# Optimization experiments

Hardware: AMD Instinct MI355X
Metric: run time of the kernel (lower is better)

The kernel has to match this reference:

```python
import jax, jax.numpy as jnp
import numpy as np

B, T, C = 32, 1024, 1024
N_LAYER, LAYER_ID, FIRST_SA = 12, 3, 1
RWKV_K_CLAMP = 60.0
RWKV_K_EPS = 1e-16


def _init_params():
    # decay_speed init exactly as in RWKV_TimeMix.__init__
    f1 = 3.0 + (LAYER_ID - FIRST_SA) / (N_LAYER - 1 - FIRST_SA) * (1.2 - 3.0)
    f2 = 0.65 + (LAYER_ID - FIRST_SA) / (N_LAYER - 1 - FIRST_SA) * (0.4 - 0.65)
    h = np.arange(C, dtype=np.float64)
    decay_speed = np.power(f2, h / (C - 1) * 7) * f1
    time_decay = np.log(decay_speed).astype(np.float32)          # (C,)
    time_first = np.full((C,), np.log(0.3), dtype=np.float32)     # (C,)
    tm = np.ones((C,), dtype=np.float32)
    tm[: C // 2] = 0.0                                            # time_mix
    return jnp.asarray(time_decay), jnp.asarray(time_first), jnp.asarray(tm)


def setup_inputs() -> dict:
    key = jax.random.key(0)
    ks = jax.random.split(key, 5)
    x = jax.random.normal(ks[0], (B, T, C), dtype=jnp.float32)
    scale = 0.02
    Wk = jax.random.normal(ks[1], (C, C), dtype=jnp.float32) * scale
    Wv = jax.random.normal(ks[2], (C, C), dtype=jnp.float32) * scale
    Wr = jax.random.normal(ks[3], (C, C), dtype=jnp.float32) * scale
    Wo = jax.random.normal(ks[4], (C, C), dtype=jnp.float32) * scale
    time_decay, time_first, time_mix = _init_params()
    return {"x": x, "time_decay": time_decay, "time_first": time_first,
            "time_mix": time_mix, "Wk": Wk, "Wv": Wv, "Wr": Wr, "Wo": Wo}


def _wkv(decay, first_w, y, eps):
    # out[b,t,c] = eps + first_w[c]*y[b,t,c] + sum_{u<t} decay[c]^(t-1-u) * y[b,u,c]
    # computed as a linear recurrence S[t] = decay*S[t-1] + y[t] via associative scan.
    a = jnp.broadcast_to(decay, y.shape)
    def comb(l, r):
        a1, b1 = l
        a2, b2 = r
        return (a1 * a2, a2 * b1 + b2)
    _, S = jax.lax.associative_scan(comb, (a, y), axis=1)
    S_prev = jnp.pad(S, ((0, 0), (1, 0), (0, 0)))[:, :-1]  # S[t-1], S[-1]=0
    return eps + first_w * y + S_prev


def reference(x, time_decay, time_first, time_mix, Wk, Wv, Wr, Wo):
    Bn, Tn, Cn = x.shape
    # time shift: ZeroPad2d((0,0,1,-1)) -> shifted[t] = x[t-1], shifted[0]=0
    xs = jnp.pad(x, ((0, 0), (1, 0), (0, 0)))[:, :-1]
    xm = x * time_mix + xs * (1.0 - time_mix)
    k = xm @ Wk.T
    v = xm @ Wv.T
    r = xm @ Wr.T
    k = jnp.exp(jnp.minimum(k, RWKV_K_CLAMP))
    kv = k * v
    decay = jnp.exp(-jnp.exp(time_decay))   # lag-d weight (d>=1): decay^(d-1)
    first_w = jnp.exp(time_first)           # lag-0 weight
    wkv = _wkv(decay, first_w, kv, 0.0)
    wk = _wkv(decay, first_w, k, RWKV_K_EPS)
    rwkv = jax.nn.sigmoid(r) * (wkv / wk)
    return rwkv @ Wo.T
```

## Files before the change

### kernel.cpp

```cpp
#include <hip/hip_runtime.h>


#define DEV __device__ __forceinline__

constexpr int Bc = 32, Tc = 1024, Cc = 1024;
constexpr int Mdim = Bc * Tc;
constexpr int Ndim = Cc;
constexpr int Kdim = Cc;
constexpr int NT = Kdim / 64;
constexpr int CHUNK = 128;
constexpr int LOOKB = 128;
constexpr int NCH = Tc / CHUNK;

typedef short bf16x8 __attribute__((ext_vector_type(8)));
typedef float f32x4  __attribute__((ext_vector_type(4)));

DEV unsigned short f2bf(float f) {
    unsigned u = __float_as_uint(f);
    u += 0x7FFFu + ((u >> 16) & 1u);
    return (unsigned short)(u >> 16);
}
DEV float bf2f(unsigned short s) { return __uint_as_float(((unsigned)s) << 16); }

DEV void gload16(const unsigned short* g, const unsigned short* l) {
    __builtin_amdgcn_global_load_lds(
        (const __attribute__((address_space(1))) void*)g,
        (__attribute__((address_space(3))) void*)l, 16, 0, 0);
}

__global__ void wconv_kernel(const float* __restrict__ src, unsigned short* __restrict__ dst) {
    int i = blockIdx.x * blockDim.x + threadIdx.x;
    float4 v = ((const float4*)src)[i];
    ((ushort4*)dst)[i] = make_ushort4(f2bf(v.x), f2bf(v.y), f2bf(v.z), f2bf(v.w));
}

__global__ void xm_kernel(const float* __restrict__ x, const float* __restrict__ tm,
                          unsigned short* __restrict__ xm) {
    int i4 = blockIdx.x * blockDim.x + threadIdx.x;
    int c4 = i4 & (Cc / 4 - 1);
    int t  = (i4 >> 8) & (Tc - 1);
    float4 xc = ((const float4*)x)[i4];
    float4 xp = make_float4(0.f, 0.f, 0.f, 0.f);
    if (t > 0) xp = ((const float4*)x)[i4 - Cc / 4];
    float4 tv = ((const float4*)tm)[c4];
    ushort4 o = make_ushort4(
        f2bf(xc.x * tv.x + xp.x * (1.f - tv.x)),
        f2bf(xc.y * tv.y + xp.y * (1.f - tv.y)),
        f2bf(xc.z * tv.z + xp.z * (1.f - tv.z)),
        f2bf(xc.w * tv.w + xp.w * (1.f - tv.w)));
    ((ushort4*)xm)[i4] = o;
}

template <int MODE>
__global__ __launch_bounds__(512, 2) void gemm256_kernel(
    const unsigned short* __restrict__ A,
    const unsigned short* __restrict__ W,
    void* __restrict__ out)
{
    __shared__ unsigned short lds[2 * 32768];

    const int tid = threadIdx.x;
    const int l = tid & 63, w = tid >> 6;
    const int wr = w >> 2, wc = w & 3;
    const int l15 = l & 15, l4 = l >> 4;
    const size_t row0 = (size_t)blockIdx.x * 256;
    const int col0 = blockIdx.y * 256;

    const int rs = tid >> 3;
    const int cs = ((tid & 7) ^ ((tid >> 3) & 7)) << 3;
    const int swz = (l15 & 7) << 3;

    f32x4 acc[8][4];
#pragma unroll
    for (int m = 0; m < 8; m++)
#pragma unroll
        for (int n = 0; n < 4; n++)
#pragma unroll
            for (int q = 0; q < 4; q++) acc[m][n][q] = 0.f;

#define STAGE(kt, bb) {                                                                \
    _Pragma("unroll")                                                                  \
    for (int g = 0; g < 4; g++)                                                        \
        gload16(A + (row0 + g * 64 + rs) * (size_t)Kdim + (kt) + cs,                   \
                lds + (bb) * 32768 + g * 4096 + w * 512);                              \
    _Pragma("unroll")                                                                  \
    for (int g = 0; g < 4; g++)                                                        \
        gload16(W + (size_t)(col0 + g * 64 + rs) * Kdim + (kt) + cs,                   \
                lds + (bb) * 32768 + 16384 + g * 4096 + w * 512); }

    STAGE(0, 0)
    asm volatile("s_waitcnt vmcnt(0)" ::: "memory");
    __builtin_amdgcn_s_barrier();

    for (int t = 0; t < NT; t++) {
        const int b = t & 1;
        const unsigned short* Ab = lds + b * 32768;
        const unsigned short* Bb = Ab + 16384;
        bf16x8 af0[4][2], af1[4][2], bf0[2][2], bf1[2][2];

#pragma unroll
        for (int mi = 0; mi < 4; mi++)
#pragma unroll
            for (int kk = 0; kk < 2; kk++)
                af0[mi][kk] = *(const bf16x8*)(Ab + (wr * 128 + mi * 16 + l15) * 64 + ((kk * 32 + l4 * 8) ^ swz));
#pragma unroll
        for (int n = 0; n < 2; n++)
#pragma unroll
            for (int kk = 0; kk < 2; kk++)
                bf0[n][kk] = *(const bf16x8*)(Bb + (wc * 64 + n * 16 + l15) * 64 + ((kk * 32 + l4 * 8) ^ swz));
        if (t < NT - 1) STAGE((t + 1) * 64, b ^ 1)
        __builtin_amdgcn_s_barrier();
        asm volatile("s_waitcnt lgkmcnt(0)" ::: "memory");
        __builtin_amdgcn_s_setprio(1);
#pragma unroll
        for (int mi = 0; mi < 4; mi++)
#pragma unroll
            for (int n = 0; n < 2; n++)
#pragma unroll
                for (int kk = 0; kk < 2; kk++)
                    acc[mi][n] = __builtin_amdgcn_mfma_f32_16x16x32_bf16(af0[mi][kk], bf0[n][kk], acc[mi][n], 0, 0, 0);
        __builtin_amdgcn_s_setprio(0);

#pragma unroll
        for (int n = 0; n < 2; n++)
#pragma unroll
            for (int kk = 0; kk < 2; kk++)
                bf1[n][kk] = *(const bf16x8*)(Bb + (wc * 64 + (2 + n) * 16 + l15) * 64 + ((kk * 32 + l4 * 8) ^ swz));
        __builtin_amdgcn_s_barrier();
        asm volatile("s_waitcnt lgkmcnt(0)" ::: "memory");
        __builtin_amdgcn_s_setprio(1);
#pragma unroll
        for (int mi = 0; mi < 4; mi++)
#pragma unroll
            for (int n = 0; n < 2; n++)
#pragma unroll
                for (int kk = 0; kk < 2; kk++)
                    acc[mi][2 + n] = __builtin_amdgcn_mfma_f32_16x16x32_bf16(af0[mi][kk], bf1[n][kk], acc[mi][2 + n], 0, 0, 0);
        __builtin_amdgcn_s_setprio(0);

#pragma unroll
        for (int mi = 0; mi < 4; mi++)
#pragma unroll
            for (int kk = 0; kk < 2; kk++)
                af1[mi][kk] = *(const bf16x8*)(Ab + (wr * 128 + (4 + mi) * 16 + l15) * 64 + ((kk * 32 + l4 * 8) ^ swz));
        __builtin_amdgcn_s_barrier();
        asm volatile("s_waitcnt lgkmcnt(0)" ::: "memory");
        __builtin_amdgcn_s_setprio(1);
#pragma unroll
        for (int mi = 0; mi < 4; mi++)
#pragma unroll
            for (int n = 0; n < 2; n++)
#pragma unroll
                for (int kk = 0; kk < 2; kk++)
                    acc[4 + mi][n] = __builtin_amdgcn_mfma_f32_16x16x32_bf16(af1[mi][kk], bf0[n][kk], acc[4 + mi][n], 0, 0, 0);
        __builtin_amdgcn_s_setprio(0);

        if (t < NT - 1) { asm volatile("s_waitcnt vmcnt(0)" ::: "memory"); }
        __builtin_amdgcn_s_barrier();
        __builtin_amdgcn_s_setprio(1);
#pragma unroll
        for (int mi = 0; mi < 4; mi++)
#pragma unroll
            for (int n = 0; n < 2; n++)
#pragma unroll
                for (int kk = 0; kk < 2; kk++)
                    acc[4 + mi][2 + n] = __builtin_amdgcn_mfma_f32_16x16x32_bf16(af1[mi][kk], bf1[n][kk], acc[4 + mi][2 + n], 0, 0, 0);
        __builtin_amdgcn_s_setprio(0);
    }
#undef STAGE

#pragma unroll
    for (int m = 0; m < 8; m++)
#pragma unroll
        for (int n = 0; n < 4; n++)
#pragma unroll
            for (int q = 0; q < 4; q++) {
                size_t row = row0 + wr * 128 + m * 16 + l4 * 4 + q;
                int col = col0 + wc * 64 + n * 16 + l15;
                size_t idx = row * Ndim + col;
                float v = acc[m][n][q];
                if constexpr (MODE == 0)
                    ((unsigned short*)out)[idx] = f2bf(__expf(fminf(v, 60.f)));
                else if constexpr (MODE == 1)
                    ((unsigned short*)out)[idx] = f2bf(v);
                else if constexpr (MODE == 2)
                    ((unsigned short*)out)[idx] = f2bf(1.f / (1.f + __expf(-v)));
                else
                    ((float*)out)[idx] = v;
            }
}

__global__ __launch_bounds__(256) void scan_kernel(
    const unsigned short* __restrict__ kexp, const unsigned short* __restrict__ vb,
    const unsigned short* __restrict__ sr,
    const float* __restrict__ td, const float* __restrict__ tf,
    unsigned short* __restrict__ rwkv)
{
    int c = blockIdx.x * blockDim.x + threadIdx.x;
    int ch = blockIdx.y;
    int b  = blockIdx.z;
    int t0 = ch * CHUNK;
    int tstart = t0 - LOOKB; if (tstart < 0) tstart = 0;

    float decay = __expf(-__expf(td[c]));
    float fw = __expf(tf[c]);
    float Skv = 0.f, Sk = 0.f;

    size_t base = (size_t)b * Tc * Cc + c;
    size_t idx = base + (size_t)tstart * Cc;
#pragma unroll 8
    for (int t = tstart; t < t0; t++, idx += Cc) {
        float kk = bf2f(kexp[idx]);
        float y  = kk * bf2f(vb[idx]);
        Skv = decay * Skv + y;
        Sk  = decay * Sk  + kk;
    }
#pragma unroll 8
    for (int t = t0; t < t0 + CHUNK; t++, idx += Cc) {
        float kk = bf2f(kexp[idx]);
        float y  = kk * bf2f(vb[idx]);
        float wkv = fw * y + Skv;
        float wk  = 1e-16f + fw * kk + Sk;
        float sig = bf2f(sr[idx]);
        rwkv[idx] = f2bf(sig * (wkv / wk));
        Skv = decay * Skv + y;
        Sk  = decay * Sk  + kk;
    }
}

extern "C" void kernel_launch(void* const* d_in, const int* in_sizes, int n_in,
                              void* d_out, int out_size, void* d_ws, size_t ws_size,
                              hipStream_t stream) {
    const float* x  = (const float*)d_in[0];
    const float* td = (const float*)d_in[1];
    const float* tf = (const float*)d_in[2];
    const float* tm = (const float*)d_in[3];
    const float* Wk = (const float*)d_in[4];
    const float* Wv = (const float*)d_in[5];
    const float* Wr = (const float*)d_in[6];
    const float* Wo = (const float*)d_in[7];

    const size_t BTC = (size_t)Bc * Tc * Cc;
    const size_t WN  = (size_t)Cc * Cc;

    char* ws = (char*)d_ws;
    unsigned short* wkb   = (unsigned short*)ws; ws += WN * 2;
    unsigned short* wvb   = (unsigned short*)ws; ws += WN * 2;
    unsigned short* wrb   = (unsigned short*)ws; ws += WN * 2;
    unsigned short* wob   = (unsigned short*)ws; ws += WN * 2;
    unsigned short* xm    = (unsigned short*)ws; ws += BTC * 2;
    unsigned short* kexpb = (unsigned short*)ws; ws += BTC * 2;
    unsigned short* vbb   = (unsigned short*)ws; ws += BTC * 2;
    unsigned short* srb   = (unsigned short*)ws; ws += BTC * 2;
    float* outp = (float*)d_out;

    wconv_kernel<<<WN / 1024, 256, 0, stream>>>(Wk, wkb);
    wconv_kernel<<<WN / 1024, 256, 0, stream>>>(Wv, wvb);
    wconv_kernel<<<WN / 1024, 256, 0, stream>>>(Wr, wrb);
    wconv_kernel<<<WN / 1024, 256, 0, stream>>>(Wo, wob);

    xm_kernel<<<BTC / 4 / 256, 256, 0, stream>>>(x, tm, xm);

    dim3 ggrid(Mdim / 256, Ndim / 256);
    gemm256_kernel<0><<<ggrid, 512, 0, stream>>>(xm, wkb, (void*)kexpb);
    gemm256_kernel<1><<<ggrid, 512, 0, stream>>>(xm, wvb, (void*)vbb);
    gemm256_kernel<2><<<ggrid, 512, 0, stream>>>(xm, wrb, (void*)srb);

    scan_kernel<<<dim3(Cc / 256, NCH, Bc), 256, 0, stream>>>(kexpb, vbb, srb, td, tf, xm);

    gemm256_kernel<3><<<ggrid, 512, 0, stream>>>(xm, wob, (void*)outp);
}
```

Before: 447.8 us.

## Merge weight conversions, swap GEMM grid order, vectorize scan to two channels per thread

Folds the four weight-conversion launches into one launch using a 2D grid. Swaps the GEMM grid so blockIdx.x walks the 4 column tiles, which means consecutive blocks share the same A row tile and should reuse it in L2. Rewrites the scan so each thread handles two adjacent channels with ushort2 loads and stores, in 64-thread blocks. The scan change widens memory accesses but doubles the register state per thread and halves the thread count.

```diff
diff --git a/kernel.cpp b/kernel.cpp
--- a/kernel.cpp
+++ b/kernel.cpp
@@ -28,8 +28,13 @@
         (__attribute__((address_space(3))) void*)l, 16, 0, 0);
 }
 
-__global__ void wconv_kernel(const float* __restrict__ src, unsigned short* __restrict__ dst) {
+__global__ void wconv_kernel(const float* __restrict__ w0, const float* __restrict__ w1,
+                             const float* __restrict__ w2, const float* __restrict__ w3,
+                             unsigned short* __restrict__ d0, unsigned short* __restrict__ d1,
+                             unsigned short* __restrict__ d2, unsigned short* __restrict__ d3) {
     int i = blockIdx.x * blockDim.x + threadIdx.x;
+    const float* src = (blockIdx.y == 0) ? w0 : (blockIdx.y == 1) ? w1 : (blockIdx.y == 2) ? w2 : w3;
+    unsigned short* dst = (blockIdx.y == 0) ? d0 : (blockIdx.y == 1) ? d1 : (blockIdx.y == 2) ? d2 : d3;
     float4 v = ((const float4*)src)[i];
     ((ushort4*)dst)[i] = make_ushort4(f2bf(v.x), f2bf(v.y), f2bf(v.z), f2bf(v.w));
 }
@@ -63,8 +68,8 @@
     const int l = tid & 63, w = tid >> 6;
     const int wr = w >> 2, wc = w & 3;
     const int l15 = l & 15, l4 = l >> 4;
-    const size_t row0 = (size_t)blockIdx.x * 256;
-    const int col0 = blockIdx.y * 256;
+    const size_t row0 = (size_t)blockIdx.y * 256;
+    const int col0 = blockIdx.x * 256;
 
     const int rs = tid >> 3;
     const int cs = ((tid & 7) ^ ((tid >> 3) & 7)) << 3;
@@ -190,41 +195,50 @@
             }
 }
 
-__global__ __launch_bounds__(256) void scan_kernel(
+__global__ __launch_bounds__(64) void scan_kernel(
     const unsigned short* __restrict__ kexp, const unsigned short* __restrict__ vb,
     const unsigned short* __restrict__ sr,
     const float* __restrict__ td, const float* __restrict__ tf,
     unsigned short* __restrict__ rwkv)
 {
-    int c = blockIdx.x * blockDim.x + threadIdx.x;
+    int c = (blockIdx.x * blockDim.x + threadIdx.x) * 2;
     int ch = blockIdx.y;
     int b  = blockIdx.z;
     int t0 = ch * CHUNK;
     int tstart = t0 - LOOKB; if (tstart < 0) tstart = 0;
 
-    float decay = __expf(-__expf(td[c]));
-    float fw = __expf(tf[c]);
-    float Skv = 0.f, Sk = 0.f;
+    float d0 = __expf(-__expf(td[c]));
+    float d1 = __expf(-__expf(td[c + 1]));
+    float f0 = __expf(tf[c]);
+    float f1 = __expf(tf[c + 1]);
+    float Skv0 = 0.f, Sk0 = 0.f, Skv1 = 0.f, Sk1 = 0.f;
 
     size_t base = (size_t)b * Tc * Cc + c;
     size_t idx = base + (size_t)tstart * Cc;
-#pragma unroll 8
+#pragma unroll 4
     for (int t = tstart; t < t0; t++, idx += Cc) {
-        float kk = bf2f(kexp[idx]);
-        float y  = kk * bf2f(vb[idx]);
-        Skv = decay * Skv + y;
-        Sk  = decay * Sk  + kk;
+        ushort2 ke = *(const ushort2*)(kexp + idx);
+        ushort2 vv = *(const ushort2*)(vb + idx);
+        float k0 = bf2f(ke.x), k1 = bf2f(ke.y);
+        float y0 = k0 * bf2f(vv.x), y1 = k1 * bf2f(vv.y);
+        Skv0 = d0 * Skv0 + y0; Sk0 = d0 * Sk0 + k0;
+        Skv1 = d1 * Skv1 + y1; Sk1 = d1 * Sk1 + k1;
     }
-#pragma unroll 8
+#pragma unroll 4
     for (int t = t0; t < t0 + CHUNK; t++, idx += Cc) {
-        float kk = bf2f(kexp[idx]);
-        float y  = kk * bf2f(vb[idx]);
-        float wkv = fw * y + Skv;
-        float wk  = 1e-16f + fw * kk + Sk;
-        float sig = bf2f(sr[idx]);
-        rwkv[idx] = f2bf(sig * (wkv / wk));
-        Skv = decay * Skv + y;
-        Sk  = decay * Sk  + kk;
+        ushort2 ke = *(const ushort2*)(kexp + idx);
+        ushort2 vv = *(const ushort2*)(vb + idx);
+        ushort2 sg = *(const ushort2*)(sr + idx);
+        float k0 = bf2f(ke.x), k1 = bf2f(ke.y);
+        float y0 = k0 * bf2f(vv.x), y1 = k1 * bf2f(vv.y);
+        float wkv0 = f0 * y0 + Skv0, wkv1 = f1 * y1 + Skv1;
+        float wk0 = 1e-16f + f0 * k0 + Sk0, wk1 = 1e-16f + f1 * k1 + Sk1;
+        ushort2 o;
+        o.x = f2bf(bf2f(sg.x) * (wkv0 / wk0));
+        o.y = f2bf(bf2f(sg.y) * (wkv1 / wk1));
+        *(ushort2*)(rwkv + idx) = o;
+        Skv0 = d0 * Skv0 + y0; Sk0 = d0 * Sk0 + k0;
+        Skv1 = d1 * Skv1 + y1; Sk1 = d1 * Sk1 + k1;
     }
 }
 
@@ -254,19 +268,16 @@
     unsigned short* srb   = (unsigned short*)ws; ws += BTC * 2;
     float* outp = (float*)d_out;
 
-    wconv_kernel<<<WN / 1024, 256, 0, stream>>>(Wk, wkb);
-    wconv_kernel<<<WN / 1024, 256, 0, stream>>>(Wv, wvb);
-    wconv_kernel<<<WN / 1024, 256, 0, stream>>>(Wr, wrb);
-    wconv_kernel<<<WN / 1024, 256, 0, stream>>>(Wo, wob);
+    wconv_kernel<<<dim3(WN / 1024, 4), 256, 0, stream>>>(Wk, Wv, Wr, Wo, wkb, wvb, wrb, wob);
 
     xm_kernel<<<BTC / 4 / 256, 256, 0, stream>>>(x, tm, xm);
 
-    dim3 ggrid(Mdim / 256, Ndim / 256);
+    dim3 ggrid(Ndim / 256, Mdim / 256);
     gemm256_kernel<0><<<ggrid, 512, 0, stream>>>(xm, wkb, (void*)kexpb);
     gemm256_kernel<1><<<ggrid, 512, 0, stream>>>(xm, wvb, (void*)vbb);
     gemm256_kernel<2><<<ggrid, 512, 0, stream>>>(xm, wrb, (void*)srb);
 
-    scan_kernel<<<dim3(Cc / 256, NCH, Bc), 256, 0, stream>>>(kexpb, vbb, srb, td, tf, xm);
+    scan_kernel<<<dim3(Cc / 128, NCH, Bc), 64, 0, stream>>>(kexpb, vbb, srb, td, tf, xm);
 
     gemm256_kernel<3><<<ggrid, 512, 0, stream>>>(xm, wob, (void*)outp);
 }
```

Result: no change. 446.3 us (-0.3%).
